# Optimization experiments

Hardware: AMD Instinct MI355X
Metric: run time of the kernel (lower is better)

Reference implementation:

```python
import jax, jax.numpy as jnp
import numpy as np
import math

B, S, H, Dh, Dr, HID, C = 2, 2048, 16, 128, 64, 2048, 512

def _linear(x, w, b):
    return x @ w.T + b

def _rope(x):
    # x: [B, H, S, Dr]; interleaved-pair rotation as in the torch module
    d = x.shape[-1]
    s = x.shape[2]
    inv_freq = 1.0 / (10000.0 ** (jnp.arange(0, d, 2, dtype=jnp.float32) / d))
    sinusoid = jnp.arange(s, dtype=jnp.float32)[:, None] * inv_freq[None, :]  # [S, d/2]
    sin, cos = jnp.sin(sinusoid), jnp.cos(sinusoid)  # broadcast over B,H
    x1 = x[..., 0::2]
    x2 = x[..., 1::2]
    rot = jnp.stack([x1 * cos - x2 * sin, x1 * sin + x2 * cos], axis=-1)
    return rot.reshape(x.shape)

def setup_inputs() -> dict:
    key = jax.random.key(0)
    ks = jax.random.split(key, 9)
    sc = 0.02
    return {
        "x": jax.random.normal(ks[0], (B, S, HID), jnp.float32),
        "d_kv_w": jax.random.normal(ks[1], (C, HID), jnp.float32) * sc,
        "d_kv_b": jnp.zeros((C,), jnp.float32),
        "u_k_w": jax.random.normal(ks[2], (H * Dh, C), jnp.float32) * sc,
        "u_k_b": jnp.zeros((H * Dh,), jnp.float32),
        "u_v_w": jax.random.normal(ks[3], (H * Dh, C), jnp.float32) * sc,
        "u_v_b": jnp.zeros((H * Dh,), jnp.float32),
        "d_q_w": jax.random.normal(ks[4], (C, HID), jnp.float32) * sc,
        "d_q_b": jnp.zeros((C,), jnp.float32),
        "u_q_w": jax.random.normal(ks[5], (H * Dh, C), jnp.float32) * sc,
        "u_q_b": jnp.zeros((H * Dh,), jnp.float32),
        "qr_w": jax.random.normal(ks[6], (H * Dr, C), jnp.float32) * sc,
        "qr_b": jnp.zeros((H * Dr,), jnp.float32),
        "out_w": jax.random.normal(ks[7], (HID, H * Dh), jnp.float32) * sc,
        "out_b": jnp.zeros((HID,), jnp.float32),
    }

def reference(x, d_kv_w, d_kv_b, u_k_w, u_k_b, u_v_w, u_v_b,
              d_q_w, d_q_b, u_q_w, u_q_b, qr_w, qr_b, out_w, out_b):
    b, s, _ = x.shape
    kv_c = _linear(x, d_kv_w, d_kv_b)                      # [B,S,C]
    k_c = _linear(kv_c, u_k_w, u_k_b).reshape(b, s, H, Dh)
    k_r = _linear(kv_c, qr_w, qr_b).reshape(b, s, H, Dr)   # note: qr_proj reused, as in source
    v = _linear(kv_c, u_v_w, u_v_b).reshape(b, s, H, Dh)
    q_c_lat = _linear(x, d_q_w, d_q_b)                     # [B,S,C]
    q_c = _linear(q_c_lat, u_q_w, u_q_b).reshape(b, s, H, Dh)
    q_r = _linear(q_c_lat, qr_w, qr_b).reshape(b, s, H, Dr)
    # RoPE operates on [B,H,S,Dr]
    q_r = _rope(q_r.transpose(0, 2, 1, 3)).transpose(0, 2, 1, 3)
    k_r = _rope(k_r.transpose(0, 2, 1, 3)).transpose(0, 2, 1, 3)
    q = jnp.concatenate([q_c, q_r], axis=-1)               # [B,S,H,Dh+Dr]
    k = jnp.concatenate([k_c, k_r], axis=-1)
    scale = 1.0 / math.sqrt(Dh + Dr)
    scores = jnp.einsum('bqhd,bkhd->bhqk', q, k) * scale   # [B,H,S,S]
    probs = jax.nn.softmax(scores, axis=-1)
    ctx = jnp.einsum('bhqk,bkhd->bqhd', probs, v).reshape(b, s, H * Dh)
    return _linear(ctx, out_w, out_b)
```

## Files before the change

### kernel.cpp

```cpp
#include <hip/hip_runtime.h>
#include <hip/hip_bf16.h>
#include <math.h>
#include <stdint.h>

#define NB 2
#define NS 2048
#define NH 16
#define NDH 128
#define NDR 64
#define NHID 2048
#define NC 512

typedef unsigned short u16;
typedef short short8 __attribute__((ext_vector_type(8)));
typedef short short4v __attribute__((ext_vector_type(4)));
typedef float f32x4 __attribute__((ext_vector_type(4)));
typedef float f32x16 __attribute__((ext_vector_type(16)));
typedef int int2v __attribute__((ext_vector_type(2)));

template <int V> struct IC { static constexpr int value = V; };

__device__ __forceinline__ u16 f2bf(float f) {
  union { float f; uint32_t u; } c; c.f = f;
  uint32_t u = c.u + 0x7fffu + ((c.u >> 16) & 1u);
  return (u16)(u >> 16);
}
__device__ __forceinline__ float bf2f(u16 b) {
  union { uint32_t u; float f; } c; c.u = ((uint32_t)b) << 16;
  return c.f;
}
__device__ __forceinline__ void async16(const void* g, void* l) {
  __builtin_amdgcn_global_load_lds((const __attribute__((address_space(1))) void*)g,
                                   (__attribute__((address_space(3))) void*)l, 16, 0, 0);
}
__device__ __forceinline__ int cvtpk(float a, float b) {
  int r;
  asm("v_cvt_pk_bf16_f32 %0, %1, %2" : "=v"(r) : "v"(a), "v"(b));
  return r;
}

struct CastArgs {
  const float* src[8];
  u16* dst[8];
  int start[8];
};

__global__ __launch_bounds__(256) void cast_kernel(CastArgs a) {
  int blk = blockIdx.x;
  int ti = 0;
#pragma unroll
  for (int i = 1; i < 8; ++i) ti += (blk >= a.start[i]) ? 1 : 0;
  size_t off = (size_t)(blk - a.start[ti]) * 2048 + (size_t)threadIdx.x * 8;
  const float4* s = (const float4*)(a.src[ti] + off);
  float4 v0 = s[0], v1 = s[1];
  u16 o[8];
  o[0] = f2bf(v0.x); o[1] = f2bf(v0.y); o[2] = f2bf(v0.z); o[3] = f2bf(v0.w);
  o[4] = f2bf(v1.x); o[5] = f2bf(v1.y); o[6] = f2bf(v1.z); o[7] = f2bf(v1.w);
  *(short8*)(a.dst[ti] + off) = *(short8*)o;
}

struct GemmSeg {
  const u16* A;
  const u16* W;
  const float* bias;
  void* dst;
  int K;
  int mode;
  int ldc;
};
struct GemmArgs {
  GemmSeg seg[5];
  int nbstart[6];
  int nseg;
};

__global__ __launch_bounds__(256) void gemm_bt(GemmArgs ga) {
  __shared__ char glds[32768];
  const int nb = blockIdx.x, mb = blockIdx.y;
  int si = 0;
  for (int i = 1; i < ga.nseg; ++i) si += (nb >= ga.nbstart[i]) ? 1 : 0;
  GemmSeg sg = ga.seg[si];
  const int nbl = nb - ga.nbstart[si];
  const int K = sg.K;
  const int t = threadIdx.x;
  const int l = t & 63, w = t >> 6;
  const int r0 = t >> 2, c0 = (t & 3) * 8;
  const int wm = (w >> 1) * 64, wn = (w & 1) * 64;
  const int frow = l & 15, fk = (l >> 4) * 8;
  const int lafO = ((wm + frow) * 32 + fk) * 2;
  const int lbfO = 8192 + ((wn + frow) * 32 + fk) * 2;

  const u16* apA = sg.A + (size_t)mb * 128 * K + (size_t)r0 * K + c0;
  const u16* wpA = sg.W + (size_t)nbl * 128 * K + (size_t)r0 * K + c0;

  auto stage = [&](int bufOff) {
    async16(apA, glds + bufOff + t * 16);
    async16(apA + (size_t)64 * K, glds + bufOff + 4096 + t * 16);
    async16(wpA, glds + bufOff + 8192 + t * 16);
    async16(wpA + (size_t)64 * K, glds + bufOff + 12288 + t * 16);
    apA += 32; wpA += 32;
  };

  const f32x4 vzero = {0.f, 0.f, 0.f, 0.f};
  f32x4 acc[4][4];
#pragma unroll
  for (int i = 0; i < 4; ++i)
#pragma unroll
    for (int j = 0; j < 4; ++j) acc[i][j] = vzero;

  stage(0);
  const int nk = K / 32;

  auto ktile = [&](auto bufc, bool stageNext) {
    constexpr int BO = decltype(bufc)::value;
    if (stageNext) {
      stage(BO ^ 16384);
      asm volatile("s_waitcnt vmcnt(4)" ::: "memory");
    } else {
      asm volatile("s_waitcnt vmcnt(0)" ::: "memory");
    }
    __builtin_amdgcn_s_barrier();
    asm volatile("" ::: "memory");
    short8 af[4], bfr[4];
#pragma unroll
    for (int i = 0; i < 4; ++i) af[i] = *(const short8*)(glds + BO + lafO + i * 1024);
#pragma unroll
    for (int j = 0; j < 4; ++j) bfr[j] = *(const short8*)(glds + BO + lbfO + j * 1024);
    __builtin_amdgcn_s_setprio(1);
#pragma unroll
    for (int i = 0; i < 4; ++i)
#pragma unroll
      for (int j = 0; j < 4; ++j)
        acc[i][j] = __builtin_amdgcn_mfma_f32_16x16x32_bf16(af[i], bfr[j], acc[i][j], 0, 0, 0);
    __builtin_amdgcn_s_setprio(0);
    asm volatile("s_waitcnt lgkmcnt(0)" ::: "memory");
    __builtin_amdgcn_s_barrier();
  };

  for (int kk = 0; kk < nk; kk += 2) {
    ktile(IC<0>{}, true);
    ktile(IC<16384>{}, kk + 2 < nk);
  }

  const int rb = (l >> 4) * 4;
  const int cl = l & 15;
  if (sg.mode == 0) {
    u16* D = (u16*)sg.dst;
#pragma unroll
    for (int i = 0; i < 4; ++i)
#pragma unroll
      for (int j = 0; j < 4; ++j) {
        int col = nbl * 128 + wn + j * 16 + cl;
        float bv = sg.bias[col];
#pragma unroll
        for (int r = 0; r < 4; ++r) {
          int row = mb * 128 + wm + i * 16 + rb + r;
          D[(size_t)row * sg.ldc + col] = f2bf(acc[i][j][r] + bv);
        }
      }
  } else if (sg.mode == 2) {
    float* D = (float*)sg.dst;
#pragma unroll
    for (int i = 0; i < 4; ++i)
#pragma unroll
      for (int j = 0; j < 4; ++j) {
        int col = nbl * 128 + wn + j * 16 + cl;
        float bv = sg.bias[col];
#pragma unroll
        for (int r = 0; r < 4; ++r) {
          int row = mb * 128 + wm + i * 16 + rb + r;
          D[(size_t)row * sg.ldc + col] = acc[i][j][r] + bv;
        }
      }
  } else {
    u16* D = (u16*)sg.dst;
#pragma unroll
    for (int i = 0; i < 4; ++i) {
      int row0 = mb * 128 + wm + i * 16 + rb;
      int bb = row0 >> 11, ss = row0 & (NS - 1);
#pragma unroll
      for (int j = 0; j < 4; ++j) {
        int col = nbl * 128 + wn + j * 16 + cl;
        int hh = col >> 7, dv = col & 127;
        float bv = sg.bias[col];
        u16 pk[4];
#pragma unroll
        for (int r = 0; r < 4; ++r) pk[r] = f2bf(acc[i][j][r] + bv);
        *(short4v*)(D + ((size_t)((bb * NH + hh) * NDH + dv)) * NS + ss) = *(short4v*)pk;
      }
    }
  }
}

__global__ __launch_bounds__(256) void rope_kernel(u16* kr, u16* qr) {
  int tid = blockIdx.x * 256 + threadIdx.x;
  int which = tid >> 19;
  int loc = tid & ((1 << 19) - 1);
  int row = loc >> 7;
  int ch = loc & 127;
  int s = row & (NS - 1);
  u16* p = (which ? qr : kr) + (size_t)row * (NH * NDR) + ch * 8;
  short8 v = *(short8*)p;
  int jb = (ch & 7) * 4;
  u16 o[8];
#pragma unroll
  for (int q = 0; q < 4; ++q) {
    int j = jb + q;
    float invf = exp2f(-(float)j * 0.41524101186f);
    float ang = (float)s * invf;
    float sn = sinf(ang), cs = cosf(ang);
    float x1 = bf2f(((u16*)&v)[2 * q]);
    float x2 = bf2f(((u16*)&v)[2 * q + 1]);
    o[2 * q]     = f2bf(x1 * cs - x2 * sn);
    o[2 * q + 1] = f2bf(x1 * sn + x2 * cs);
  }
  *(short8*)p = *(short8*)o;
}

__global__ __launch_bounds__(256, 2) void attn_kernel(
    const u16* __restrict__ Qc, const u16* __restrict__ Qr,
    const u16* __restrict__ Kc, const u16* __restrict__ Kr,
    const u16* __restrict__ VT, u16* __restrict__ Ctx) {
  extern __shared__ char smem[];
  const int t = threadIdx.x, w = t >> 6, l = t & 63;
  const int hi = l >> 5, q32 = l & 31;
  const int lin = blockIdx.x;
  const int xcd = lin & 7, idx = lin >> 3;
  const int bh = xcd * 4 + (idx >> 4);
  const int qb = idx & 15;
  const int b = bh >> 4, h = bh & 15;
  const int q0 = qb * 128 + w * 32;

  short8 qf[12];
  {
    const u16* qcp = Qc + ((size_t)(b * NS + q0 + q32)) * NHID + h * NDH + hi * 8;
    const u16* qrp = Qr + ((size_t)(b * NS + q0 + q32)) * (NH * NDR) + h * NDR + hi * 8;
#pragma unroll
    for (int dw = 0; dw < 8; ++dw) qf[dw] = *(const short8*)(qcp + dw * 16);
#pragma unroll
    for (int dw = 0; dw < 4; ++dw) qf[8 + dw] = *(const short8*)(qrp + dw * 16);
  }
#pragma unroll
  for (int dw = 0; dw < 12; ++dw) asm volatile("" :: "v"(qf[dw]));

  const u16* kptr[6]; int kstep[6];
#pragma unroll
  for (int r = 0; r < 6; ++r) {
    int Lb = r * 4096 + t * 16;
    int row = Lb / 384;
    int off = Lb - row * 384;
    int c = (off ^ ((row & 7) << 4)) >> 1;
    if (c < NDH) { kptr[r] = Kc + ((size_t)(b * NS + row)) * NHID + h * NDH + c; kstep[r] = 64 * NHID; }
    else { kptr[r] = Kr + ((size_t)(b * NS + row)) * (NH * NDR) + h * NDR + (c - NDH); kstep[r] = 64 * NH * NDR; }
  }
  const u16* vptr[4];
#pragma unroll
  for (int r = 0; r < 4; ++r) {
    int Lb = r * 4096 + t * 16;
    int row = Lb >> 7, off = Lb & 127;
    int c = (off ^ ((row & 7) << 4)) >> 1;
    vptr[r] = VT + ((size_t)(bh * NDH + row)) * NS + c;
  }

  const int kswz = (l & 7) << 4;
  float m2 = -1e30f, lsum = 0.f;
  f32x16 acc[4];
#pragma unroll
  for (int i = 0; i < 4; ++i)
#pragma unroll
    for (int r = 0; r < 16; ++r) acc[i][r] = 0.f;
  const float scale2 = 0.10411757f;

  auto stage_into = [&](int bufOff) {
#pragma unroll
    for (int r = 0; r < 6; ++r) { async16(kptr[r], smem + bufOff + r * 4096 + t * 16); kptr[r] += kstep[r]; }
#pragma unroll
    for (int r = 0; r < 4; ++r) { async16(vptr[r], smem + bufOff + 24576 + r * 4096 + t * 16); vptr[r] += 64; }
  };
  stage_into(0);

  auto tile = [&](auto bufc, bool stageNext) {
    constexpr int BO = decltype(bufc)::value;
    if (stageNext) {
      stage_into(BO ^ 40960);
      asm volatile("s_waitcnt vmcnt(10)" ::: "memory");
    } else {
      asm volatile("s_waitcnt vmcnt(0)" ::: "memory");
    }
    __builtin_amdgcn_s_barrier();
    asm volatile("" ::: "memory");

    f32x16 sa[2];
#pragma unroll
    for (int n = 0; n < 2; ++n)
#pragma unroll
      for (int r = 0; r < 16; ++r) sa[n][r] = 0.f;
#pragma unroll
    for (int dw = 0; dw < 12; ++dw) {
      int ko = q32 * 384 + ((dw * 32 + hi * 16) ^ kswz);
      short8 k0 = *(const short8*)(smem + BO + ko);
      short8 k1 = *(const short8*)(smem + BO + 12288 + ko);
      __builtin_amdgcn_s_setprio(1);
      sa[0] = __builtin_amdgcn_mfma_f32_32x32x16_bf16(k0, qf[dw], sa[0], 0, 0, 0);
      sa[1] = __builtin_amdgcn_mfma_f32_32x32x16_bf16(k1, qf[dw], sa[1], 0, 0, 0);
      __builtin_amdgcn_s_setprio(0);
    }

    float mx = sa[0][0];
#pragma unroll
    for (int r = 1; r < 16; ++r) mx = fmaxf(mx, sa[0][r]);
#pragma unroll
    for (int r = 0; r < 16; ++r) mx = fmaxf(mx, sa[1][r]);
    mx = fmaxf(mx, __shfl_xor(mx, 32));
    float mxs = mx * scale2;
    if (!__all(mxs <= m2 + 6.0f)) {
      float mn = fmaxf(m2, mxs);
      float sf = exp2f(m2 - mn);
      m2 = mn;
      lsum *= sf;
#pragma unroll
      for (int i = 0; i < 4; ++i) acc[i] *= sf;
    }
    float nm = -m2;
    float ps = 0.f;
#pragma unroll
    for (int n = 0; n < 2; ++n)
#pragma unroll
      for (int r = 0; r < 16; ++r) {
        float p = exp2f(fmaf(sa[n][r], scale2, nm));
        sa[n][r] = p;
        ps += p;
      }
    ps += __shfl_xor(ps, 32);
    lsum += ps;

#pragma unroll
    for (int n = 0; n < 2; ++n) {
#pragma unroll
      for (int w2 = 0; w2 < 2; ++w2) {
        const int base = w2 * 8;
        int A0 = cvtpk(sa[n][base + 0], sa[n][base + 1]);
        int A1 = cvtpk(sa[n][base + 2], sa[n][base + 3]);
        int B0 = cvtpk(sa[n][base + 4], sa[n][base + 5]);
        int B1 = cvtpk(sa[n][base + 6], sa[n][base + 7]);
        int2v r02 = __builtin_amdgcn_permlane32_swap(A0, B0, false, false);
        int2v r13 = __builtin_amdgcn_permlane32_swap(A1, B1, false, false);
        union { int i[4]; short8 s; } F;
        F.i[0] = r02[0]; F.i[1] = r13[0]; F.i[2] = r02[1]; F.i[3] = r13[1];
        const int W = n * 2 + w2;
        const int vo = q32 * 128 + ((W * 32 + hi * 16) ^ kswz);
        __builtin_amdgcn_s_setprio(1);
#pragma unroll
        for (int d32 = 0; d32 < 4; ++d32) {
          short8 va = *(const short8*)(smem + BO + 24576 + d32 * 4096 + vo);
          acc[d32] = __builtin_amdgcn_mfma_f32_32x32x16_bf16(va, F.s, acc[d32], 0, 0, 0);
        }
        __builtin_amdgcn_s_setprio(0);
      }
    }

    asm volatile("s_waitcnt lgkmcnt(0)" ::: "memory");
    __builtin_amdgcn_s_barrier();
  };

  for (int kv = 0; kv < NS / 64; kv += 2) {
    tile(IC<0>{}, true);
    tile(IC<40960>{}, kv + 2 < NS / 64);
  }

  float invq = 1.f / lsum;
  u16* dst = Ctx + ((size_t)(b * NS + q0 + q32)) * NHID + h * NDH + hi * 4;
#pragma unroll
  for (int d32 = 0; d32 < 4; ++d32)
#pragma unroll
    for (int m2x = 0; m2x < 4; ++m2x) {
      float a0 = acc[d32][m2x * 4 + 0] * invq, a1 = acc[d32][m2x * 4 + 1] * invq;
      float a2 = acc[d32][m2x * 4 + 2] * invq, a3 = acc[d32][m2x * 4 + 3] * invq;
      union { int i[2]; short4v s; } pu;
      pu.i[0] = cvtpk(a0, a1);
      pu.i[1] = cvtpk(a2, a3);
      *(short4v*)(dst + d32 * 32 + m2x * 8) = pu.s;
    }
}

extern "C" void kernel_launch(void* const* d_in, const int* in_sizes, int n_in,
                              void* d_out, int out_size, void* d_ws, size_t ws_size,
                              hipStream_t stream) {
  (void)in_sizes; (void)n_in; (void)out_size;
  const float* x      = (const float*)d_in[0];
  const float* d_kv_w = (const float*)d_in[1];
  const float* d_kv_b = (const float*)d_in[2];
  const float* u_k_w  = (const float*)d_in[3];
  const float* u_k_b  = (const float*)d_in[4];
  const float* u_v_w  = (const float*)d_in[5];
  const float* u_v_b  = (const float*)d_in[6];
  const float* d_q_w  = (const float*)d_in[7];
  const float* d_q_b  = (const float*)d_in[8];
  const float* u_q_w  = (const float*)d_in[9];
  const float* u_q_b  = (const float*)d_in[10];
  const float* qr_w   = (const float*)d_in[11];
  const float* qr_b   = (const float*)d_in[12];
  const float* out_w  = (const float*)d_in[13];
  const float* out_b  = (const float*)d_in[14];

  char* ws = (char*)d_ws;
  size_t off = 0;
  auto alloc = [&](size_t bytes) -> void* {
    void* p = ws + off;
    off += (bytes + 255) & ~(size_t)255;
    return p;
  };
  u16* xb   = (u16*)alloc((size_t)NB * NS * NHID * 2);
  u16* wdkv = (u16*)alloc((size_t)NC * NHID * 2);
  u16* wuk  = (u16*)alloc((size_t)NH * NDH * NC * 2);
  u16* wuv  = (u16*)alloc((size_t)NH * NDH * NC * 2);
  u16* wdq  = (u16*)alloc((size_t)NC * NHID * 2);
  u16* wuq  = (u16*)alloc((size_t)NH * NDH * NC * 2);
  u16* wqr  = (u16*)alloc((size_t)NH * NDR * NC * 2);
  u16* wout = (u16*)alloc((size_t)NHID * NH * NDH * 2);
  u16* kvc  = (u16*)alloc((size_t)NB * NS * NC * 2);
  u16* qlat = (u16*)alloc((size_t)NB * NS * NC * 2);
  u16* Kc   = (u16*)alloc((size_t)NB * NS * NH * NDH * 2);
  u16* Krt  = (u16*)alloc((size_t)NB * NS * NH * NDR * 2);
  u16* Qc   = (u16*)alloc((size_t)NB * NS * NH * NDH * 2);
  u16* Qrt  = (u16*)alloc((size_t)NB * NS * NH * NDR * 2);
  u16* VT   = (u16*)alloc((size_t)NB * NH * NDH * NS * 2);
  u16* ctx  = xb;
  if (off > ws_size) return;

  {
    CastArgs ca;
    const float* srcs[8] = {x, d_kv_w, u_k_w, u_v_w, d_q_w, u_q_w, qr_w, out_w};
    u16* dsts[8] = {xb, wdkv, wuk, wuv, wdq, wuq, wqr, wout};
    int sizes[8] = {NB * NS * NHID, NC * NHID, NH * NDH * NC, NH * NDH * NC,
                    NC * NHID, NH * NDH * NC, NH * NDR * NC, NHID * NH * NDH};
    int st = 0;
    for (int i = 0; i < 8; ++i) {
      ca.src[i] = srcs[i]; ca.dst[i] = dsts[i]; ca.start[i] = st;
      st += sizes[i] / 2048;
    }
    cast_kernel<<<dim3(st), dim3(256), 0, stream>>>(ca);
  }

  {
    GemmArgs ga;
    ga.nseg = 2;
    ga.seg[0] = {xb, wdkv, d_kv_b, kvc, NHID, 0, NC};
    ga.seg[1] = {xb, wdq,  d_q_b,  qlat, NHID, 0, NC};
    for (int i = 2; i < 5; ++i) ga.seg[i] = ga.seg[0];
    ga.nbstart[0] = 0; ga.nbstart[1] = 4; ga.nbstart[2] = 8;
    ga.nbstart[3] = 8; ga.nbstart[4] = 8; ga.nbstart[5] = 8;
    gemm_bt<<<dim3(8, 32), dim3(256), 0, stream>>>(ga);
  }

  {
    GemmArgs ga;
    ga.nseg = 5;
    ga.seg[0] = {kvc,  wuk, u_k_b, Kc,  NC, 0, NH * NDH};
    ga.seg[1] = {kvc,  wuv, u_v_b, VT,  NC, 1, 0};
    ga.seg[2] = {kvc,  wqr, qr_b,  Krt, NC, 0, NH * NDR};
    ga.seg[3] = {qlat, wuq, u_q_b, Qc,  NC, 0, NH * NDH};
    ga.seg[4] = {qlat, wqr, qr_b,  Qrt, NC, 0, NH * NDR};
    ga.nbstart[0] = 0;  ga.nbstart[1] = 16; ga.nbstart[2] = 32;
    ga.nbstart[3] = 40; ga.nbstart[4] = 56; ga.nbstart[5] = 64;
    gemm_bt<<<dim3(64, 32), dim3(256), 0, stream>>>(ga);
  }

  rope_kernel<<<dim3(4096), dim3(256), 0, stream>>>(Krt, Qrt);

  hipFuncSetAttribute((const void*)attn_kernel,
                      hipFuncAttributeMaxDynamicSharedMemorySize, 81920);
  attn_kernel<<<dim3(512), dim3(256), 81920, stream>>>(Qc, Qrt, Kc, Krt, VT, ctx);

  {
    GemmArgs ga;
    ga.nseg = 1;
    ga.seg[0] = {ctx, wout, out_b, d_out, NHID, 2, NHID};
    for (int i = 1; i < 5; ++i) ga.seg[i] = ga.seg[0];
    ga.nbstart[0] = 0;
    for (int i = 1; i < 6; ++i) ga.nbstart[i] = 16;
    gemm_bt<<<dim3(16, 32), dim3(256), 0, stream>>>(ga);
  }
}
```

Before: 280.5 us.

## Fuse RoPE into projection GEMM epilogue and pre-tile K/V for attention

Removes the separate RoPE kernel by applying the rotation in the GEMM epilogue, using a lane shuffle to pair each even and odd element. K (content plus rotary) and V are written in a blocked 8-element layout, so the attention kernel can stage them with simple contiguous async loads and read LDS without XOR swizzling. The first down-projection GEMM now runs with 8 waves per block (512 threads). The risks are extra sin/cos work in the epilogue, scattered 2-byte stores in the new write modes, and possible LDS bank conflicts now that the swizzle is gone.

```diff
diff --git a/kernel.cpp b/kernel.cpp
--- a/kernel.cpp
+++ b/kernel.cpp
@@ -74,7 +74,10 @@
   int nseg;
 };
 
-__global__ __launch_bounds__(256) void gemm_bt(GemmArgs ga) {
+template <int NW>
+__global__ __launch_bounds__(NW * 64) void gemm_bt(GemmArgs ga) {
+  constexpr int NT = NW * 64;
+  constexpr int NJ = (NW == 8) ? 2 : 4;
   __shared__ char glds[32768];
   const int nb = blockIdx.x, mb = blockIdx.y;
   int si = 0;
@@ -85,7 +88,8 @@
   const int t = threadIdx.x;
   const int l = t & 63, w = t >> 6;
   const int r0 = t >> 2, c0 = (t & 3) * 8;
-  const int wm = (w >> 1) * 64, wn = (w & 1) * 64;
+  const int wm = (NW == 8 ? (w >> 2) : (w >> 1)) * 64;
+  const int wn = (NW == 8) ? (w & 3) * 32 : (w & 1) * 64;
   const int frow = l & 15, fk = (l >> 4) * 8;
   const int lafO = ((wm + frow) * 32 + fk) * 2;
   const int lbfO = 8192 + ((wn + frow) * 32 + fk) * 2;
@@ -94,19 +98,24 @@
   const u16* wpA = sg.W + (size_t)nbl * 128 * K + (size_t)r0 * K + c0;
 
   auto stage = [&](int bufOff) {
-    async16(apA, glds + bufOff + t * 16);
-    async16(apA + (size_t)64 * K, glds + bufOff + 4096 + t * 16);
-    async16(wpA, glds + bufOff + 8192 + t * 16);
-    async16(wpA + (size_t)64 * K, glds + bufOff + 12288 + t * 16);
+    if constexpr (NT == 512) {
+      async16(apA, glds + bufOff + t * 16);
+      async16(wpA, glds + bufOff + 8192 + t * 16);
+    } else {
+      async16(apA, glds + bufOff + t * 16);
+      async16(apA + (size_t)64 * K, glds + bufOff + 4096 + t * 16);
+      async16(wpA, glds + bufOff + 8192 + t * 16);
+      async16(wpA + (size_t)64 * K, glds + bufOff + 12288 + t * 16);
+    }
     apA += 32; wpA += 32;
   };
 
   const f32x4 vzero = {0.f, 0.f, 0.f, 0.f};
-  f32x4 acc[4][4];
+  f32x4 acc[4][NJ];
 #pragma unroll
   for (int i = 0; i < 4; ++i)
 #pragma unroll
-    for (int j = 0; j < 4; ++j) acc[i][j] = vzero;
+    for (int j = 0; j < NJ; ++j) acc[i][j] = vzero;
 
   stage(0);
   const int nk = K / 32;
@@ -115,22 +124,25 @@
     constexpr int BO = decltype(bufc)::value;
     if (stageNext) {
       stage(BO ^ 16384);
-      asm volatile("s_waitcnt vmcnt(4)" ::: "memory");
+      if constexpr (NT == 512)
+        asm volatile("s_waitcnt vmcnt(2)" ::: "memory");
+      else
+        asm volatile("s_waitcnt vmcnt(4)" ::: "memory");
     } else {
       asm volatile("s_waitcnt vmcnt(0)" ::: "memory");
     }
     __builtin_amdgcn_s_barrier();
     asm volatile("" ::: "memory");
-    short8 af[4], bfr[4];
+    short8 af[4], bfr[NJ];
 #pragma unroll
     for (int i = 0; i < 4; ++i) af[i] = *(const short8*)(glds + BO + lafO + i * 1024);
 #pragma unroll
-    for (int j = 0; j < 4; ++j) bfr[j] = *(const short8*)(glds + BO + lbfO + j * 1024);
+    for (int j = 0; j < NJ; ++j) bfr[j] = *(const short8*)(glds + BO + lbfO + j * 1024);
     __builtin_amdgcn_s_setprio(1);
 #pragma unroll
     for (int i = 0; i < 4; ++i)
 #pragma unroll
-      for (int j = 0; j < 4; ++j)
+      for (int j = 0; j < NJ; ++j)
         acc[i][j] = __builtin_amdgcn_mfma_f32_16x16x32_bf16(af[i], bfr[j], acc[i][j], 0, 0, 0);
     __builtin_amdgcn_s_setprio(0);
     asm volatile("s_waitcnt lgkmcnt(0)" ::: "memory");
@@ -144,12 +156,13 @@
 
   const int rb = (l >> 4) * 4;
   const int cl = l & 15;
-  if (sg.mode == 0) {
+  const int mode = sg.mode;
+  if (mode == 0) {
     u16* D = (u16*)sg.dst;
 #pragma unroll
     for (int i = 0; i < 4; ++i)
 #pragma unroll
-      for (int j = 0; j < 4; ++j) {
+      for (int j = 0; j < NJ; ++j) {
         int col = nbl * 128 + wn + j * 16 + cl;
         float bv = sg.bias[col];
 #pragma unroll
@@ -158,12 +171,12 @@
           D[(size_t)row * sg.ldc + col] = f2bf(acc[i][j][r] + bv);
         }
       }
-  } else if (sg.mode == 2) {
+  } else if (mode == 2) {
     float* D = (float*)sg.dst;
 #pragma unroll
     for (int i = 0; i < 4; ++i)
 #pragma unroll
-      for (int j = 0; j < 4; ++j) {
+      for (int j = 0; j < NJ; ++j) {
         int col = nbl * 128 + wn + j * 16 + cl;
         float bv = sg.bias[col];
 #pragma unroll
@@ -172,55 +185,98 @@
           D[(size_t)row * sg.ldc + col] = acc[i][j][r] + bv;
         }
       }
-  } else {
+  } else if (mode == 1) {
     u16* D = (u16*)sg.dst;
 #pragma unroll
     for (int i = 0; i < 4; ++i) {
       int row0 = mb * 128 + wm + i * 16 + rb;
-      int bb = row0 >> 11, ss = row0 & (NS - 1);
-#pragma unroll
-      for (int j = 0; j < 4; ++j) {
+      int bb = row0 >> 11, s = row0 & (NS - 1);
+#pragma unroll
+      for (int j = 0; j < NJ; ++j) {
         int col = nbl * 128 + wn + j * 16 + cl;
         int hh = col >> 7, dv = col & 127;
         float bv = sg.bias[col];
         u16 pk[4];
 #pragma unroll
         for (int r = 0; r < 4; ++r) pk[r] = f2bf(acc[i][j][r] + bv);
-        *(short4v*)(D + ((size_t)((bb * NH + hh) * NDH + dv)) * NS + ss) = *(short4v*)pk;
-      }
-    }
-  }
-}
-
-__global__ __launch_bounds__(256) void rope_kernel(u16* kr, u16* qr) {
-  int tid = blockIdx.x * 256 + threadIdx.x;
-  int which = tid >> 19;
-  int loc = tid & ((1 << 19) - 1);
-  int row = loc >> 7;
-  int ch = loc & 127;
-  int s = row & (NS - 1);
-  u16* p = (which ? qr : kr) + (size_t)row * (NH * NDR) + ch * 8;
-  short8 v = *(short8*)p;
-  int jb = (ch & 7) * 4;
-  u16 o[8];
-#pragma unroll
-  for (int q = 0; q < 4; ++q) {
-    int j = jb + q;
-    float invf = exp2f(-(float)j * 0.41524101186f);
-    float ang = (float)s * invf;
-    float sn = sinf(ang), cs = cosf(ang);
-    float x1 = bf2f(((u16*)&v)[2 * q]);
-    float x2 = bf2f(((u16*)&v)[2 * q + 1]);
-    o[2 * q]     = f2bf(x1 * cs - x2 * sn);
-    o[2 * q + 1] = f2bf(x1 * sn + x2 * cs);
-  }
-  *(short8*)p = *(short8*)o;
+        size_t cell = ((size_t)((bb * NH + hh) * (NS / 8) + (s >> 3)) * 128 + dv) * 8 + (s & 7);
+        *(short4v*)(D + cell) = *(short4v*)pk;
+      }
+    }
+  } else if (mode == 4) {
+    u16* D = (u16*)sg.dst;
+#pragma unroll
+    for (int i = 0; i < 4; ++i) {
+      int row0 = mb * 128 + wm + i * 16 + rb;
+      int bb = row0 >> 11, s = row0 & (NS - 1);
+#pragma unroll
+      for (int j = 0; j < NJ; ++j) {
+        int col = nbl * 128 + wn + j * 16 + cl;
+        int hh = col >> 7, d = col & 127;
+        float bv = sg.bias[col];
+        size_t base = ((size_t)((bb * NH + hh) * 24 + (d >> 3)) * NS + s) * 8 + (d & 7);
+#pragma unroll
+        for (int r = 0; r < 4; ++r) D[base + r * 8] = f2bf(acc[i][j][r] + bv);
+      }
+    }
+  } else if (mode == 5) {
+    u16* D = (u16*)sg.dst;
+#pragma unroll
+    for (int i = 0; i < 4; ++i) {
+      int row0 = mb * 128 + wm + i * 16 + rb;
+      int bb = row0 >> 11, s = row0 & (NS - 1);
+#pragma unroll
+      for (int j = 0; j < NJ; ++j) {
+        int col = nbl * 128 + wn + j * 16 + cl;
+        int hh = col >> 6, dr = col & 63;
+        int jp = dr >> 1;
+        bool ev = !(dr & 1);
+        float invf = exp2f(-(float)jp * 0.41524101186f);
+        float bv = sg.bias[col];
+        size_t base = ((size_t)((bb * NH + hh) * 24 + 16 + (dr >> 3)) * NS + s) * 8 + (dr & 7);
+#pragma unroll
+        for (int r = 0; r < 4; ++r) {
+          float v = acc[i][j][r] + bv;
+          float p = __shfl_xor(v, 1);
+          float ang = (float)(s + r) * invf;
+          float sn = sinf(ang), cs = cosf(ang);
+          float out = ev ? (v * cs - p * sn) : (p * sn + v * cs);
+          D[base + r * 8] = f2bf(out);
+        }
+      }
+    }
+  } else {
+    u16* D = (u16*)sg.dst;
+#pragma unroll
+    for (int i = 0; i < 4; ++i) {
+      int row0 = mb * 128 + wm + i * 16 + rb;
+      int s = row0 & (NS - 1);
+#pragma unroll
+      for (int j = 0; j < NJ; ++j) {
+        int col = nbl * 128 + wn + j * 16 + cl;
+        int dr = col & 63;
+        int jp = dr >> 1;
+        bool ev = !(dr & 1);
+        float invf = exp2f(-(float)jp * 0.41524101186f);
+        float bv = sg.bias[col];
+#pragma unroll
+        for (int r = 0; r < 4; ++r) {
+          float v = acc[i][j][r] + bv;
+          float p = __shfl_xor(v, 1);
+          float ang = (float)(s + r) * invf;
+          float sn = sinf(ang), cs = cosf(ang);
+          float out = ev ? (v * cs - p * sn) : (p * sn + v * cs);
+          D[(size_t)(row0 + r) * sg.ldc + col] = f2bf(out);
+        }
+      }
+    }
+  }
 }
 
 __global__ __launch_bounds__(256, 2) void attn_kernel(
     const u16* __restrict__ Qc, const u16* __restrict__ Qr,
-    const u16* __restrict__ Kc, const u16* __restrict__ Kr,
-    const u16* __restrict__ VT, u16* __restrict__ Ctx) {
+    const u16* __restrict__ Ktb, const u16* __restrict__ Vtb,
+    u16* __restrict__ Ctx) {
   extern __shared__ char smem[];
   const int t = threadIdx.x, w = t >> 6, l = t & 63;
   const int hi = l >> 5, q32 = l & 31;
@@ -243,26 +299,16 @@
 #pragma unroll
   for (int dw = 0; dw < 12; ++dw) asm volatile("" :: "v"(qf[dw]));
 
-  const u16* kptr[6]; int kstep[6];
-#pragma unroll
-  for (int r = 0; r < 6; ++r) {
-    int Lb = r * 4096 + t * 16;
-    int row = Lb / 384;
-    int off = Lb - row * 384;
-    int c = (off ^ ((row & 7) << 4)) >> 1;
-    if (c < NDH) { kptr[r] = Kc + ((size_t)(b * NS + row)) * NHID + h * NDH + c; kstep[r] = 64 * NHID; }
-    else { kptr[r] = Kr + ((size_t)(b * NS + row)) * (NH * NDR) + h * NDR + (c - NDH); kstep[r] = 64 * NH * NDR; }
-  }
-  const u16* vptr[4];
-#pragma unroll
-  for (int r = 0; r < 4; ++r) {
-    int Lb = r * 4096 + t * 16;
-    int row = Lb >> 7, off = Lb & 127;
-    int c = (off ^ ((row & 7) << 4)) >> 1;
-    vptr[r] = VT + ((size_t)(bh * NDH + row)) * NS + c;
-  }
-
-  const int kswz = (l & 7) << 4;
+  const int w2 = t >> 6;
+  const u16* kp[6];
+#pragma unroll
+  for (int r = 0; r < 6; ++r)
+    kp[r] = Ktb + ((size_t)(bh * 24 + r * 4 + w2) * NS + l) * 8;
+  const u16* vp = Vtb + (size_t)bh * NS * 128 + t * 8;
+
+  const int kbase = q32 * 16 + hi * 1024;
+  const int vbase = 24576 + q32 * 16 + hi * 2048;
+
   float m2 = -1e30f, lsum = 0.f;
   f32x16 acc[4];
 #pragma unroll
@@ -273,9 +319,10 @@
 
   auto stage_into = [&](int bufOff) {
 #pragma unroll
-    for (int r = 0; r < 6; ++r) { async16(kptr[r], smem + bufOff + r * 4096 + t * 16); kptr[r] += kstep[r]; }
-#pragma unroll
-    for (int r = 0; r < 4; ++r) { async16(vptr[r], smem + bufOff + 24576 + r * 4096 + t * 16); vptr[r] += 64; }
+    for (int r = 0; r < 6; ++r) { async16(kp[r], smem + bufOff + r * 4096 + t * 16); kp[r] += 512; }
+#pragma unroll
+    for (int r = 0; r < 4; ++r) async16(vp + r * 2048, smem + bufOff + 24576 + r * 4096 + t * 16);
+    vp += 8192;
   };
   stage_into(0);
 
@@ -297,9 +344,8 @@
       for (int r = 0; r < 16; ++r) sa[n][r] = 0.f;
 #pragma unroll
     for (int dw = 0; dw < 12; ++dw) {
-      int ko = q32 * 384 + ((dw * 32 + hi * 16) ^ kswz);
-      short8 k0 = *(const short8*)(smem + BO + ko);
-      short8 k1 = *(const short8*)(smem + BO + 12288 + ko);
+      short8 k0 = *(const short8*)(smem + BO + kbase + dw * 2048);
+      short8 k1 = *(const short8*)(smem + BO + kbase + dw * 2048 + 512);
       __builtin_amdgcn_s_setprio(1);
       sa[0] = __builtin_amdgcn_mfma_f32_32x32x16_bf16(k0, qf[dw], sa[0], 0, 0, 0);
       sa[1] = __builtin_amdgcn_mfma_f32_32x32x16_bf16(k1, qf[dw], sa[1], 0, 0, 0);
@@ -337,8 +383,8 @@
 #pragma unroll
     for (int n = 0; n < 2; ++n) {
 #pragma unroll
-      for (int w2 = 0; w2 < 2; ++w2) {
-        const int base = w2 * 8;
+      for (int w2i = 0; w2i < 2; ++w2i) {
+        const int base = w2i * 8;
         int A0 = cvtpk(sa[n][base + 0], sa[n][base + 1]);
         int A1 = cvtpk(sa[n][base + 2], sa[n][base + 3]);
         int B0 = cvtpk(sa[n][base + 4], sa[n][base + 5]);
@@ -347,12 +393,11 @@
         int2v r13 = __builtin_amdgcn_permlane32_swap(A1, B1, false, false);
         union { int i[4]; short8 s; } F;
         F.i[0] = r02[0]; F.i[1] = r13[0]; F.i[2] = r02[1]; F.i[3] = r13[1];
-        const int W = n * 2 + w2;
-        const int vo = q32 * 128 + ((W * 32 + hi * 16) ^ kswz);
+        const int W = n * 2 + w2i;
         __builtin_amdgcn_s_setprio(1);
 #pragma unroll
         for (int d32 = 0; d32 < 4; ++d32) {
-          short8 va = *(const short8*)(smem + BO + 24576 + d32 * 4096 + vo);
+          short8 va = *(const short8*)(smem + BO + vbase + W * 4096 + d32 * 512);
           acc[d32] = __builtin_amdgcn_mfma_f32_32x32x16_bf16(va, F.s, acc[d32], 0, 0, 0);
         }
         __builtin_amdgcn_s_setprio(0);
@@ -420,11 +465,10 @@
   u16* wout = (u16*)alloc((size_t)NHID * NH * NDH * 2);
   u16* kvc  = (u16*)alloc((size_t)NB * NS * NC * 2);
   u16* qlat = (u16*)alloc((size_t)NB * NS * NC * 2);
-  u16* Kc   = (u16*)alloc((size_t)NB * NS * NH * NDH * 2);
-  u16* Krt  = (u16*)alloc((size_t)NB * NS * NH * NDR * 2);
+  u16* Ktb  = (u16*)alloc((size_t)NB * NH * 24 * NS * 8 * 2);
+  u16* Vtb  = (u16*)alloc((size_t)NB * NH * NS * NDH * 2);
   u16* Qc   = (u16*)alloc((size_t)NB * NS * NH * NDH * 2);
   u16* Qrt  = (u16*)alloc((size_t)NB * NS * NH * NDR * 2);
-  u16* VT   = (u16*)alloc((size_t)NB * NH * NDH * NS * 2);
   u16* ctx  = xb;
   if (off > ws_size) return;
 
@@ -450,27 +494,25 @@
     for (int i = 2; i < 5; ++i) ga.seg[i] = ga.seg[0];
     ga.nbstart[0] = 0; ga.nbstart[1] = 4; ga.nbstart[2] = 8;
     ga.nbstart[3] = 8; ga.nbstart[4] = 8; ga.nbstart[5] = 8;
-    gemm_bt<<<dim3(8, 32), dim3(256), 0, stream>>>(ga);
+    gemm_bt<8><<<dim3(8, 32), dim3(512), 0, stream>>>(ga);
   }
 
   {
     GemmArgs ga;
     ga.nseg = 5;
-    ga.seg[0] = {kvc,  wuk, u_k_b, Kc,  NC, 0, NH * NDH};
-    ga.seg[1] = {kvc,  wuv, u_v_b, VT,  NC, 1, 0};
-    ga.seg[2] = {kvc,  wqr, qr_b,  Krt, NC, 0, NH * NDR};
+    ga.seg[0] = {kvc,  wuk, u_k_b, Ktb, NC, 4, 0};
+    ga.seg[1] = {kvc,  wuv, u_v_b, Vtb, NC, 1, 0};
+    ga.seg[2] = {kvc,  wqr, qr_b,  Ktb, NC, 5, 0};
     ga.seg[3] = {qlat, wuq, u_q_b, Qc,  NC, 0, NH * NDH};
-    ga.seg[4] = {qlat, wqr, qr_b,  Qrt, NC, 0, NH * NDR};
+    ga.seg[4] = {qlat, wqr, qr_b,  Qrt, NC, 3, NH * NDR};
     ga.nbstart[0] = 0;  ga.nbstart[1] = 16; ga.nbstart[2] = 32;
     ga.nbstart[3] = 40; ga.nbstart[4] = 56; ga.nbstart[5] = 64;
-    gemm_bt<<<dim3(64, 32), dim3(256), 0, stream>>>(ga);
-  }
-
-  rope_kernel<<<dim3(4096), dim3(256), 0, stream>>>(Krt, Qrt);
+    gemm_bt<4><<<dim3(64, 32), dim3(256), 0, stream>>>(ga);
+  }
 
   hipFuncSetAttribute((const void*)attn_kernel,
                       hipFuncAttributeMaxDynamicSharedMemorySize, 81920);
-  attn_kernel<<<dim3(512), dim3(256), 81920, stream>>>(Qc, Qrt, Kc, Krt, VT, ctx);
+  attn_kernel<<<dim3(512), dim3(256), 81920, stream>>>(Qc, Qrt, Ktb, Vtb, ctx);
 
   {
     GemmArgs ga;
@@ -479,6 +521,6 @@
     for (int i = 1; i < 5; ++i) ga.seg[i] = ga.seg[0];
     ga.nbstart[0] = 0;
     for (int i = 1; i < 6; ++i) ga.nbstart[i] = 16;
-    gemm_bt<<<dim3(16, 32), dim3(256), 0, stream>>>(ga);
-  }
-}
+    gemm_bt<4><<<dim3(16, 32), dim3(256), 0, stream>>>(ga);
+  }
+}
```

New measurement: 323.8 us. 1.15x slower.
